# Optimization experiments

Hardware: AMD Instinct MI355X
Metric: run time of the kernel (lower is better)

Reference implementation:

```python
import jax, jax.numpy as jnp
import numpy as np


def setup_inputs() -> dict:
    key = jax.random.key(0)
    x = jax.random.normal(key, (8192, 4096), dtype=jnp.float32)
    return {"x": x, "k": 1}


def reference(x, k):
    # torch.linalg.svdvals returns singular values in descending order;
    # jnp.linalg.svd with compute_uv=False does the same.
    s = jnp.linalg.svd(x, compute_uv=False)  # [min(m, n)], descending
    return jnp.sum(s[:k] ** 2)
```

## Files before the change

kernel.cpp:

```cpp
#include <hip/hip_runtime.h>
#include <hip/hip_fp16.h>
#include <math.h>


#define NROWS 8192
#define NCOLS 4096
#define T_STEPS 16
#define BMV_BLOCKS 512
#define RPC 8

__global__ __launch_bounds__(256) void init_kernel(float* __restrict__ ws) {
    int i = blockIdx.x * 256 + threadIdx.x;
    float* r1 = ws;
    float* r0 = ws + 4096;
    float* slots = ws + 12288;
    unsigned h = (unsigned)i * 2654435761u;
    h ^= h >> 16; h *= 2246822519u; h ^= h >> 13;
    r1[i] = (h & 1u) ? 0.015625f : -0.015625f;
    r0[i] = 0.f;
    if (i < 128) slots[i] = (i == 64 || i == 65) ? 1.f : 0.f;
}

__global__ __launch_bounds__(256) void convert_kernel(const float* __restrict__ A,
                                                      __half* __restrict__ Ah) {
    const float4* A4 = (const float4*)A;
    float2* O2 = (float2*)Ah;
    for (int i = blockIdx.x * 256 + threadIdx.x; i < (NROWS * NCOLS / 4); i += 2048 * 256) {
        float4 f = A4[i];
        union { float2 f2; __half2 h2[2]; } u;
        u.h2[0] = __halves2half2(__float2half_rn(f.x), __float2half_rn(f.y));
        u.h2[1] = __halves2half2(__float2half_rn(f.z), __float2half_rn(f.w));
        O2[i] = u.f2;
    }
}

__device__ __forceinline__ void up8(const float4& p, float* f) {
    const __half2* h = (const __half2*)&p;
    float2 t0 = __half22float2(h[0]);
    float2 t1 = __half22float2(h[1]);
    float2 t2 = __half22float2(h[2]);
    float2 t3 = __half22float2(h[3]);
    f[0] = t0.x; f[1] = t0.y; f[2] = t1.x; f[3] = t1.y;
    f[4] = t2.x; f[5] = t2.y; f[6] = t3.x; f[7] = t3.y;
}

__global__ __launch_bounds__(256, 4) void bmv(const __half* __restrict__ Ah,
                                              const float* __restrict__ rc,
                                              float* __restrict__ partials,
                                              float* __restrict__ slots,
                                              int j) {
    __shared__ float s_lds[RPC];
    int tid = threadIdx.x, lane = tid & 63;
    float inv = rsqrtf(fmaxf(slots[64 + j], 1e-30f));
    int cA = tid * 8, cB = 2048 + tid * 8;
    float vA[8], vB[8];
    {
        const float4* r4 = (const float4*)(rc + cA);
        float4 x = r4[0], y = r4[1];
        vA[0] = x.x * inv; vA[1] = x.y * inv; vA[2] = x.z * inv; vA[3] = x.w * inv;
        vA[4] = y.x * inv; vA[5] = y.y * inv; vA[6] = y.z * inv; vA[7] = y.w * inv;
        const float4* s4 = (const float4*)(rc + cB);
        float4 z = s4[0], w = s4[1];
        vB[0] = z.x * inv; vB[1] = z.y * inv; vB[2] = z.z * inv; vB[3] = z.w * inv;
        vB[4] = w.x * inv; vB[5] = w.y * inv; vB[6] = w.z * inv; vB[7] = w.w * inv;
    }
    float wacc[16];
#pragma unroll
    for (int i = 0; i < 16; ++i) wacc[i] = 0.f;

#pragma unroll 1
    for (int ch = 0; ch < 2; ++ch) {
        int row0 = ch * 4096 + blockIdx.x * RPC;
        const __half* base = Ah + (size_t)row0 * NCOLS;
        float4 alo[RPC], ahi[RPC];
#pragma unroll
        for (int r = 0; r < RPC; ++r) {
            alo[r] = *(const float4*)(base + (size_t)r * NCOLS + cA);
            ahi[r] = *(const float4*)(base + (size_t)r * NCOLS + cB);
        }
        __syncthreads();
        if (tid < RPC) s_lds[tid] = 0.f;
        __syncthreads();
#pragma unroll
        for (int r = 0; r < RPC; ++r) {
            float f[8];
            up8(alo[r], f);
            float sp = f[0] * vA[0] + f[1] * vA[1] + f[2] * vA[2] + f[3] * vA[3]
                     + f[4] * vA[4] + f[5] * vA[5] + f[6] * vA[6] + f[7] * vA[7];
            up8(ahi[r], f);
            sp += f[0] * vB[0] + f[1] * vB[1] + f[2] * vB[2] + f[3] * vB[3]
                + f[4] * vB[4] + f[5] * vB[5] + f[6] * vB[6] + f[7] * vB[7];
#pragma unroll
            for (int off = 32; off > 0; off >>= 1) sp += __shfl_xor(sp, off);
            if (lane == 0) atomicAdd(&s_lds[r], sp);
        }
        __syncthreads();
        if (tid == 0) {
            float aa = 0.f;
#pragma unroll
            for (int r = 0; r < RPC; ++r) aa += s_lds[r] * s_lds[r];
            atomicAdd(&slots[j], aa);
        }
#pragma unroll
        for (int r = 0; r < RPC; ++r) {
            float s = s_lds[r];
            float f[8];
            up8(alo[r], f);
            wacc[0] += s * f[0]; wacc[1] += s * f[1]; wacc[2] += s * f[2]; wacc[3] += s * f[3];
            wacc[4] += s * f[4]; wacc[5] += s * f[5]; wacc[6] += s * f[6]; wacc[7] += s * f[7];
            up8(ahi[r], f);
            wacc[8] += s * f[0]; wacc[9] += s * f[1]; wacc[10] += s * f[2]; wacc[11] += s * f[3];
            wacc[12] += s * f[4]; wacc[13] += s * f[5]; wacc[14] += s * f[6]; wacc[15] += s * f[7];
        }
    }
    float* pb = partials + (size_t)blockIdx.x * NCOLS;
    float4* pa = (float4*)(pb + cA);
    pa[0] = make_float4(wacc[0], wacc[1], wacc[2], wacc[3]);
    pa[1] = make_float4(wacc[4], wacc[5], wacc[6], wacc[7]);
    float4* pc = (float4*)(pb + cB);
    pc[0] = make_float4(wacc[8], wacc[9], wacc[10], wacc[11]);
    pc[1] = make_float4(wacc[12], wacc[13], wacc[14], wacc[15]);
}

__global__ __launch_bounds__(256) void red1(const float* __restrict__ partials,
                                            float* __restrict__ p2) {
    int cb = blockIdx.x >> 5, g = blockIdx.x & 31;
    int col = cb * 256 + threadIdx.x;
    const float* p = partials + (size_t)(g * 16) * NCOLS + col;
    float s = 0.f;
#pragma unroll
    for (int k = 0; k < 16; ++k) s += p[(size_t)k * NCOLS];
    p2[(size_t)g * NCOLS + col] = s;
}

__global__ __launch_bounds__(256) void red2(const float* __restrict__ p2,
                                            float* __restrict__ wt,
                                            const float* __restrict__ rc,
                                            const float* __restrict__ rp,
                                            float* __restrict__ slots,
                                            int j) {
    int tid = threadIdx.x;
    int col = blockIdx.x * 256 + tid;
    float w = 0.f;
#pragma unroll
    for (int g = 0; g < 32; ++g) w += p2[(size_t)g * NCOLS + col];
    float a = slots[j];
    float n2j = fmaxf(slots[64 + j], 1e-30f);
    float n2m = fmaxf(slots[64 + j - 1], 1e-30f);
    float invj = rsqrtf(n2j);
    float cb = sqrtf(n2j / n2m);
    float rn = w - a * invj * rc[col] - cb * rp[col];
    wt[col] = rn;
    float p = rn * rn;
#pragma unroll
    for (int off = 32; off > 0; off >>= 1) p += __shfl_xor(p, off);
    __shared__ float part[4];
    int lane = tid & 63, wq = tid >> 6;
    if (lane == 0) part[wq] = p;
    __syncthreads();
    if (tid == 0)
        atomicAdd(&slots[64 + j + 1], part[0] + part[1] + part[2] + part[3]);
}

__global__ void solve_kernel(const float* __restrict__ slots,
                             float* __restrict__ out, int t) {
    __shared__ float d_s[64], e2_s[64];
    int lane = threadIdx.x;
    d_s[lane] = (lane < t) ? slots[1 + lane] : 0.f;
    e2_s[lane] = (lane < t - 1) ? slots[64 + lane + 2] : 0.f;
    __syncthreads();
    float e_here = sqrtf(e2_s[lane]);
    float e_prev = (lane > 0) ? sqrtf(e2_s[lane - 1]) : 0.f;
    float d = d_s[lane];
    float gersh = (lane < t) ? d + e_here + e_prev : 0.f;
    float dmax = (lane < t) ? d : 0.f;
#pragma unroll
    for (int off = 32; off > 0; off >>= 1) {
        gersh = fmaxf(gersh, __shfl_xor(gersh, off));
        dmax = fmaxf(dmax, __shfl_xor(dmax, off));
    }
    float lo = dmax, hi = gersh + 1e-3f;
    for (int round = 0; round < 3; ++round) {
        float stepw = (hi - lo) * (1.f / 64.f);
        float x = lo + stepw * (lane + 1);
        double qv = 1.0;
        int cnt = 0;
        for (int i = 0; i < t; ++i) {
            double qi = (double)d_s[i] - (double)x - ((i > 0) ? (double)e2_s[i - 1] / qv : 0.0);
            if (fabs(qi) < 1e-300) qi = -1e-300;
            cnt += (qi < 0.0);
            qv = qi;
        }
        unsigned long long m = __ballot(cnt < t);
        if (m) {
            int h = 63 - __clzll(m);
            lo = lo + stepw * (h + 1);
            hi = lo + stepw;
        } else {
            hi = lo + stepw;
        }
    }
    if (lane == 0) out[0] = 0.5f * (lo + hi);
}

extern "C" void kernel_launch(void* const* d_in, const int* in_sizes, int n_in,
                              void* d_out, int out_size, void* d_ws, size_t ws_size,
                              hipStream_t stream) {
    const float* A = (const float*)d_in[0];
    float* out = (float*)d_out;
    float* ws = (float*)d_ws;
    float* vb[3] = {ws, ws + 4096, ws + 8192};
    float* slots = ws + 12288;
    float* p2 = ws + 16384;
    float* partials = ws + 262144;
    __half* Ah = (__half*)((char*)d_ws + (size_t)16 * 1024 * 1024);

    init_kernel<<<16, 256, 0, stream>>>(ws);
    convert_kernel<<<2048, 256, 0, stream>>>(A, Ah);

    const int T = T_STEPS;
    for (int j = 1; j <= T; ++j) {
        float* rc = vb[j % 3];
        float* rp = vb[(j + 2) % 3];
        float* wt = vb[(j + 1) % 3];
        bmv<<<BMV_BLOCKS, 256, 0, stream>>>(Ah, rc, partials, slots, j);
        if (j < T) {
            red1<<<512, 256, 0, stream>>>(partials, p2);
            red2<<<16, 256, 0, stream>>>(p2, wt, rc, rp, slots, j);
        }
    }
    solve_kernel<<<1, 64, 0, stream>>>(slots, out, T);
}
```

Before: 844.3 us.

## Fuse Lanczos reductions into one kernel and cut iteration count

Lanczos steps drop from 16 to 14. The two-stage red1/red2 reduction becomes a single red_kernel. The bmv kernel now computes the vector norm itself and writes per-row dot products to a buffer instead of doing global atomics for alpha. When the workspace is large enough it launches 1024 blocks with 8 rows each, so every block loads its rows once; otherwise it uses 512 blocks processing two 8-row batches. This cuts launch count and atomic traffic per iteration, but fewer iterations could lower the accuracy of the top singular value estimate.

```diff
diff --git a/kernel.cpp b/kernel.cpp
--- a/kernel.cpp
+++ b/kernel.cpp
@@ -5,20 +5,15 @@
 
 #define NROWS 8192
 #define NCOLS 4096
-#define T_STEPS 16
-#define BMV_BLOCKS 512
-#define RPC 8
+#define T_STEPS 14
 
 __global__ __launch_bounds__(256) void init_kernel(float* __restrict__ ws) {
     int i = blockIdx.x * 256 + threadIdx.x;
-    float* r1 = ws;
-    float* r0 = ws + 4096;
-    float* slots = ws + 12288;
     unsigned h = (unsigned)i * 2654435761u;
     h ^= h >> 16; h *= 2246822519u; h ^= h >> 13;
-    r1[i] = (h & 1u) ? 0.015625f : -0.015625f;
-    r0[i] = 0.f;
-    if (i < 128) slots[i] = (i == 64 || i == 65) ? 1.f : 0.f;
+    ws[4096 + i] = (h & 1u) ? 0.015625f : -0.015625f;
+    ws[i] = 0.f;
+    if (i < 128) ws[12288 + i] = (i == 64) ? 1.f : 0.f;
 }
 
 __global__ __launch_bounds__(256) void convert_kernel(const float* __restrict__ A,
@@ -28,13 +23,13 @@
     for (int i = blockIdx.x * 256 + threadIdx.x; i < (NROWS * NCOLS / 4); i += 2048 * 256) {
         float4 f = A4[i];
         union { float2 f2; __half2 h2[2]; } u;
-        u.h2[0] = __halves2half2(__float2half_rn(f.x), __float2half_rn(f.y));
-        u.h2[1] = __halves2half2(__float2half_rn(f.z), __float2half_rn(f.w));
+        u.h2[0] = __floats2half2_rn(f.x, f.y);
+        u.h2[1] = __floats2half2_rn(f.z, f.w);
         O2[i] = u.f2;
     }
 }
 
-__device__ __forceinline__ void up8(const float4& p, float* f) {
+__device__ __forceinline__ void dec8(const float4& p, float* f) {
     const __half2* h = (const __half2*)&p;
     float2 t0 = __half22float2(h[0]);
     float2 t1 = __half22float2(h[1]);
@@ -44,129 +39,154 @@
     f[4] = t2.x; f[5] = t2.y; f[6] = t3.x; f[7] = t3.y;
 }
 
+template <int RPB>
 __global__ __launch_bounds__(256, 4) void bmv(const __half* __restrict__ Ah,
                                               const float* __restrict__ rc,
                                               float* __restrict__ partials,
+                                              float* __restrict__ su,
                                               float* __restrict__ slots,
                                               int j) {
-    __shared__ float s_lds[RPC];
-    int tid = threadIdx.x, lane = tid & 63;
-    float inv = rsqrtf(fmaxf(slots[64 + j], 1e-30f));
-    int cA = tid * 8, cB = 2048 + tid * 8;
+    __shared__ float dgrid[4][8];
+    __shared__ float s_lds[8];
+    __shared__ float red4[4];
+    const int tid = threadIdx.x, lane = tid & 63, wv = tid >> 6;
+    const int b = blockIdx.x;
+    const int cA = tid * 8, cB = 2048 + tid * 8;
+
     float vA[8], vB[8];
     {
-        const float4* r4 = (const float4*)(rc + cA);
-        float4 x = r4[0], y = r4[1];
-        vA[0] = x.x * inv; vA[1] = x.y * inv; vA[2] = x.z * inv; vA[3] = x.w * inv;
-        vA[4] = y.x * inv; vA[5] = y.y * inv; vA[6] = y.z * inv; vA[7] = y.w * inv;
-        const float4* s4 = (const float4*)(rc + cB);
-        float4 z = s4[0], w = s4[1];
-        vB[0] = z.x * inv; vB[1] = z.y * inv; vB[2] = z.z * inv; vB[3] = z.w * inv;
-        vB[4] = w.x * inv; vB[5] = w.y * inv; vB[6] = w.z * inv; vB[7] = w.w * inv;
-    }
+        const float4* ra = (const float4*)(rc + cA);
+        float4 x = ra[0], y = ra[1];
+        const float4* rb = (const float4*)(rc + cB);
+        float4 z = rb[0], w = rb[1];
+        vA[0]=x.x; vA[1]=x.y; vA[2]=x.z; vA[3]=x.w;
+        vA[4]=y.x; vA[5]=y.y; vA[6]=y.z; vA[7]=y.w;
+        vB[0]=z.x; vB[1]=z.y; vB[2]=z.z; vB[3]=z.w;
+        vB[4]=w.x; vB[5]=w.y; vB[6]=w.z; vB[7]=w.w;
+    }
+    float nn = 0.f;
+#pragma unroll
+    for (int i = 0; i < 8; ++i) nn += vA[i] * vA[i] + vB[i] * vB[i];
+#pragma unroll
+    for (int off = 32; off; off >>= 1) nn += __shfl_xor(nn, off);
+    if (lane == 0) red4[wv] = nn;
+    __syncthreads();
+    float norm2 = red4[0] + red4[1] + red4[2] + red4[3];
+    if (b == 0 && tid == 0) slots[64 + j] = norm2;
+    float inv = rsqrtf(fmaxf(norm2, 1e-30f));
+#pragma unroll
+    for (int i = 0; i < 8; ++i) { vA[i] *= inv; vB[i] *= inv; }
+
     float wacc[16];
 #pragma unroll
     for (int i = 0; i < 16; ++i) wacc[i] = 0.f;
+    const __half* sl = Ah + (size_t)b * RPB * NCOLS;
 
 #pragma unroll 1
-    for (int ch = 0; ch < 2; ++ch) {
-        int row0 = ch * 4096 + blockIdx.x * RPC;
-        const __half* base = Ah + (size_t)row0 * NCOLS;
-        float4 alo[RPC], ahi[RPC];
-#pragma unroll
-        for (int r = 0; r < RPC; ++r) {
-            alo[r] = *(const float4*)(base + (size_t)r * NCOLS + cA);
-            ahi[r] = *(const float4*)(base + (size_t)r * NCOLS + cB);
+    for (int batch = 0; batch < RPB / 8; ++batch) {
+        float4 alo[8], ahi[8];
+#pragma unroll
+        for (int r = 0; r < 8; ++r) {
+            const __half* rowp = sl + (size_t)(batch * 8 + r) * NCOLS;
+            alo[r] = *(const float4*)(rowp + cA);
+            ahi[r] = *(const float4*)(rowp + cB);
+        }
+        float sp[8];
+#pragma unroll
+        for (int r = 0; r < 8; ++r) {
+            float f[8];
+            dec8(alo[r], f);
+            float s = f[0]*vA[0]+f[1]*vA[1]+f[2]*vA[2]+f[3]*vA[3]
+                    + f[4]*vA[4]+f[5]*vA[5]+f[6]*vA[6]+f[7]*vA[7];
+            dec8(ahi[r], f);
+            s += f[0]*vB[0]+f[1]*vB[1]+f[2]*vB[2]+f[3]*vB[3]
+               + f[4]*vB[4]+f[5]*vB[5]+f[6]*vB[6]+f[7]*vB[7];
+            sp[r] = s;
+        }
+#pragma unroll
+        for (int r = 0; r < 8; ++r) {
+#pragma unroll
+            for (int off = 32; off; off >>= 1) sp[r] += __shfl_xor(sp[r], off);
+        }
+        if (batch) __syncthreads();
+        if (lane == 0) {
+#pragma unroll
+            for (int r = 0; r < 8; ++r) dgrid[wv][r] = sp[r];
         }
         __syncthreads();
-        if (tid < RPC) s_lds[tid] = 0.f;
+        if (tid < 8) {
+            float s = dgrid[0][tid] + dgrid[1][tid] + dgrid[2][tid] + dgrid[3][tid];
+            s_lds[tid] = s;
+            su[b * RPB + batch * 8 + tid] = s;
+        }
         __syncthreads();
 #pragma unroll
-        for (int r = 0; r < RPC; ++r) {
-            float f[8];
-            up8(alo[r], f);
-            float sp = f[0] * vA[0] + f[1] * vA[1] + f[2] * vA[2] + f[3] * vA[3]
-                     + f[4] * vA[4] + f[5] * vA[5] + f[6] * vA[6] + f[7] * vA[7];
-            up8(ahi[r], f);
-            sp += f[0] * vB[0] + f[1] * vB[1] + f[2] * vB[2] + f[3] * vB[3]
-                + f[4] * vB[4] + f[5] * vB[5] + f[6] * vB[6] + f[7] * vB[7];
-#pragma unroll
-            for (int off = 32; off > 0; off >>= 1) sp += __shfl_xor(sp, off);
-            if (lane == 0) atomicAdd(&s_lds[r], sp);
-        }
-        __syncthreads();
-        if (tid == 0) {
-            float aa = 0.f;
-#pragma unroll
-            for (int r = 0; r < RPC; ++r) aa += s_lds[r] * s_lds[r];
-            atomicAdd(&slots[j], aa);
-        }
-#pragma unroll
-        for (int r = 0; r < RPC; ++r) {
+        for (int r = 0; r < 8; ++r) {
             float s = s_lds[r];
             float f[8];
-            up8(alo[r], f);
-            wacc[0] += s * f[0]; wacc[1] += s * f[1]; wacc[2] += s * f[2]; wacc[3] += s * f[3];
-            wacc[4] += s * f[4]; wacc[5] += s * f[5]; wacc[6] += s * f[6]; wacc[7] += s * f[7];
-            up8(ahi[r], f);
-            wacc[8] += s * f[0]; wacc[9] += s * f[1]; wacc[10] += s * f[2]; wacc[11] += s * f[3];
-            wacc[12] += s * f[4]; wacc[13] += s * f[5]; wacc[14] += s * f[6]; wacc[15] += s * f[7];
-        }
-    }
-    float* pb = partials + (size_t)blockIdx.x * NCOLS;
-    float4* pa = (float4*)(pb + cA);
-    pa[0] = make_float4(wacc[0], wacc[1], wacc[2], wacc[3]);
-    pa[1] = make_float4(wacc[4], wacc[5], wacc[6], wacc[7]);
-    float4* pc = (float4*)(pb + cB);
-    pc[0] = make_float4(wacc[8], wacc[9], wacc[10], wacc[11]);
-    pc[1] = make_float4(wacc[12], wacc[13], wacc[14], wacc[15]);
-}
-
-__global__ __launch_bounds__(256) void red1(const float* __restrict__ partials,
-                                            float* __restrict__ p2) {
-    int cb = blockIdx.x >> 5, g = blockIdx.x & 31;
-    int col = cb * 256 + threadIdx.x;
-    const float* p = partials + (size_t)(g * 16) * NCOLS + col;
-    float s = 0.f;
-#pragma unroll
-    for (int k = 0; k < 16; ++k) s += p[(size_t)k * NCOLS];
-    p2[(size_t)g * NCOLS + col] = s;
-}
-
-__global__ __launch_bounds__(256) void red2(const float* __restrict__ p2,
-                                            float* __restrict__ wt,
-                                            const float* __restrict__ rc,
-                                            const float* __restrict__ rp,
-                                            float* __restrict__ slots,
-                                            int j) {
-    int tid = threadIdx.x;
-    int col = blockIdx.x * 256 + tid;
-    float w = 0.f;
-#pragma unroll
-    for (int g = 0; g < 32; ++g) w += p2[(size_t)g * NCOLS + col];
-    float a = slots[j];
-    float n2j = fmaxf(slots[64 + j], 1e-30f);
-    float n2m = fmaxf(slots[64 + j - 1], 1e-30f);
-    float invj = rsqrtf(n2j);
-    float cb = sqrtf(n2j / n2m);
-    float rn = w - a * invj * rc[col] - cb * rp[col];
-    wt[col] = rn;
-    float p = rn * rn;
-#pragma unroll
-    for (int off = 32; off > 0; off >>= 1) p += __shfl_xor(p, off);
-    __shared__ float part[4];
-    int lane = tid & 63, wq = tid >> 6;
-    if (lane == 0) part[wq] = p;
+            dec8(alo[r], f);
+            wacc[0]+=s*f[0]; wacc[1]+=s*f[1]; wacc[2]+=s*f[2]; wacc[3]+=s*f[3];
+            wacc[4]+=s*f[4]; wacc[5]+=s*f[5]; wacc[6]+=s*f[6]; wacc[7]+=s*f[7];
+            dec8(ahi[r], f);
+            wacc[8]+=s*f[0]; wacc[9]+=s*f[1]; wacc[10]+=s*f[2]; wacc[11]+=s*f[3];
+            wacc[12]+=s*f[4]; wacc[13]+=s*f[5]; wacc[14]+=s*f[6]; wacc[15]+=s*f[7];
+        }
+    }
+    float* pb_ = partials + (size_t)b * NCOLS;
+    float4* w4 = (float4*)(pb_ + cA);
+    w4[0] = make_float4(wacc[0], wacc[1], wacc[2], wacc[3]);
+    w4[1] = make_float4(wacc[4], wacc[5], wacc[6], wacc[7]);
+    float4* w5 = (float4*)(pb_ + cB);
+    w5[0] = make_float4(wacc[8], wacc[9], wacc[10], wacc[11]);
+    w5[1] = make_float4(wacc[12], wacc[13], wacc[14], wacc[15]);
+}
+
+__global__ __launch_bounds__(256) void red_kernel(const float* __restrict__ partials,
+                                                  const float* __restrict__ su,
+                                                  float* __restrict__ wt,
+                                                  const float* __restrict__ rc,
+                                                  const float* __restrict__ rp,
+                                                  float* __restrict__ slots,
+                                                  int j, int NP) {
+    __shared__ float redw[4][64];
+    __shared__ float red4[4];
+    int tid = threadIdx.x, lane = tid & 63, wv = tid >> 6;
+    int col = blockIdx.x * 64 + lane;
+    float aa = 0.f;
+    for (int k = tid; k < NROWS; k += 256) { float s = su[k]; aa += s * s; }
+#pragma unroll
+    for (int off = 32; off; off >>= 1) aa += __shfl_xor(aa, off);
+    if (lane == 0) red4[wv] = aa;
+    float wsum = 0.f;
+    int q = NP >> 2;
+    const float* p0 = partials + (size_t)(wv * q) * NCOLS + col;
+    for (int g = 0; g < q; ++g) wsum += p0[(size_t)g * NCOLS];
+    redw[wv][lane] = wsum;
     __syncthreads();
-    if (tid == 0)
-        atomicAdd(&slots[64 + j + 1], part[0] + part[1] + part[2] + part[3]);
+    if (tid < 64) {
+        float alpha = red4[0] + red4[1] + red4[2] + red4[3];
+        if (blockIdx.x == 0 && tid == 0) slots[j] = alpha;
+        int c = blockIdx.x * 64 + tid;
+        float w = redw[0][tid] + redw[1][tid] + redw[2][tid] + redw[3][tid];
+        float n2j = fmaxf(slots[64 + j], 1e-30f);
+        float n2m = fmaxf(slots[64 + j - 1], 1e-30f);
+        float invj = rsqrtf(n2j);
+        float cb = sqrtf(n2j / n2m);
+        wt[c] = w - alpha * invj * rc[c] - cb * rp[c];
+    }
 }
 
 __global__ void solve_kernel(const float* __restrict__ slots,
+                             const float* __restrict__ su,
                              float* __restrict__ out, int t) {
+    int lane = threadIdx.x;
+    float aa = 0.f;
+    for (int k = lane; k < NROWS; k += 64) { float s = su[k]; aa += s * s; }
+#pragma unroll
+    for (int off = 32; off; off >>= 1) aa += __shfl_xor(aa, off);
+    float alphaT = aa;
     __shared__ float d_s[64], e2_s[64];
-    int lane = threadIdx.x;
-    d_s[lane] = (lane < t) ? slots[1 + lane] : 0.f;
+    d_s[lane] = (lane < t - 1) ? slots[1 + lane] : ((lane == t - 1) ? alphaT : 0.f);
     e2_s[lane] = (lane < t - 1) ? slots[64 + lane + 2] : 0.f;
     __syncthreads();
     float e_here = sqrtf(e2_s[lane]);
@@ -175,7 +195,7 @@
     float gersh = (lane < t) ? d + e_here + e_prev : 0.f;
     float dmax = (lane < t) ? d : 0.f;
 #pragma unroll
-    for (int off = 32; off > 0; off >>= 1) {
+    for (int off = 32; off; off >>= 1) {
         gersh = fmaxf(gersh, __shfl_xor(gersh, off));
         dmax = fmaxf(dmax, __shfl_xor(dmax, off));
     }
@@ -186,15 +206,16 @@
         double qv = 1.0;
         int cnt = 0;
         for (int i = 0; i < t; ++i) {
-            double qi = (double)d_s[i] - (double)x - ((i > 0) ? (double)e2_s[i - 1] / qv : 0.0);
+            double qi = (double)d_s[i] - (double)x -
+                        ((i > 0) ? (double)e2_s[i - 1] / qv : 0.0);
             if (fabs(qi) < 1e-300) qi = -1e-300;
             cnt += (qi < 0.0);
             qv = qi;
         }
         unsigned long long m = __ballot(cnt < t);
         if (m) {
-            int h = 63 - __clzll(m);
-            lo = lo + stepw * (h + 1);
+            int hbit = 63 - __clzll(m);
+            lo = lo + stepw * (hbit + 1);
             hi = lo + stepw;
         } else {
             hi = lo + stepw;
@@ -211,9 +232,13 @@
     float* ws = (float*)d_ws;
     float* vb[3] = {ws, ws + 4096, ws + 8192};
     float* slots = ws + 12288;
-    float* p2 = ws + 16384;
-    float* partials = ws + 262144;
+    float* su = ws + 12416;
     __half* Ah = (__half*)((char*)d_ws + (size_t)16 * 1024 * 1024);
+
+    const size_t MiB = 1024 * 1024;
+    bool big = ws_size >= 97 * MiB;
+    int NP = big ? 1024 : 512;
+    float* partials = big ? (float*)((char*)d_ws + 80 * MiB) : (ws + 24576);
 
     init_kernel<<<16, 256, 0, stream>>>(ws);
     convert_kernel<<<2048, 256, 0, stream>>>(A, Ah);
@@ -223,11 +248,12 @@
         float* rc = vb[j % 3];
         float* rp = vb[(j + 2) % 3];
         float* wt = vb[(j + 1) % 3];
-        bmv<<<BMV_BLOCKS, 256, 0, stream>>>(Ah, rc, partials, slots, j);
-        if (j < T) {
-            red1<<<512, 256, 0, stream>>>(partials, p2);
-            red2<<<16, 256, 0, stream>>>(p2, wt, rc, rp, slots, j);
-        }
-    }
-    solve_kernel<<<1, 64, 0, stream>>>(slots, out, T);
-}
+        if (big)
+            bmv<8><<<1024, 256, 0, stream>>>(Ah, rc, partials, su, slots, j);
+        else
+            bmv<16><<<512, 256, 0, stream>>>(Ah, rc, partials, su, slots, j);
+        if (j < T)
+            red_kernel<<<64, 256, 0, stream>>>(partials, su, wt, rc, rp, slots, j, NP);
+    }
+    solve_kernel<<<1, 64, 0, stream>>>(slots, su, out, T);
+}
```

After: 1.533 ms. 81.6% more time.
